# Performance work log

Hardware: AMD Instinct MI355X
Metric: run time of the kernel (lower is better)

Reference implementation:

```python
import jax, jax.numpy as jnp
import numpy as np

DILATION = 3
HC_MULT = 4
HIDDEN_DIM = 32
ENGRAM_DIM = 32
KERNEL_SIZE = 4
EPS = 1.1920929e-07  # torch RMSNorm default eps=None -> finfo(fp32).eps


def rmsnorm(x, w):
    # x: [..., C], w broadcastable to x
    ms = jnp.mean(x * x, axis=-1, keepdims=True)
    return x * jax.lax.rsqrt(ms + EPS) * w


def setup_inputs() -> dict:
    key = jax.random.key(0)
    ks = jax.random.split(key, 12)
    B, T = 16, 8192
    s = 0.05
    return {
        "embeddings": jax.random.normal(ks[0], (B, T, ENGRAM_DIM), jnp.float32),
        "hidden_states": jax.random.normal(ks[1], (B, T, HC_MULT, HIDDEN_DIM), jnp.float32),
        "Wv": jax.random.normal(ks[2], (HIDDEN_DIM, ENGRAM_DIM), jnp.float32) * s,
        "bv": jax.random.normal(ks[3], (HIDDEN_DIM,), jnp.float32) * s,
        "Wk": jax.random.normal(ks[4], (HC_MULT, HIDDEN_DIM, ENGRAM_DIM), jnp.float32) * s,
        "bk": jax.random.normal(ks[5], (HC_MULT, HIDDEN_DIM), jnp.float32) * s,
        "n1_w": jnp.ones((HC_MULT, HIDDEN_DIM), jnp.float32),
        "n2_w": jnp.ones((HC_MULT, HIDDEN_DIM), jnp.float32),
        "cn_w": jnp.ones((HC_MULT, HIDDEN_DIM), jnp.float32),
        "conv_w": jax.random.normal(ks[6], (HC_MULT * HIDDEN_DIM, 1, KERNEL_SIZE), jnp.float32) * s,
    }


def reference(embeddings, hidden_states, Wv, bv, Wk, bk, n1_w, n2_w, cn_w, conv_w):
    B, T, G, C = hidden_states.shape
    # per-branch key projection: [B,T,G,C]
    key = jnp.einsum("btd,gcd->btgc", embeddings, Wk) + bk
    normed_key = rmsnorm(key, n1_w)                    # [B,T,G,C]
    normed_query = rmsnorm(hidden_states, n2_w)        # [B,T,G,C]
    gate = jnp.sum(normed_key * normed_query, axis=-1) / np.sqrt(C)  # [B,T,G]
    gate = jnp.sqrt(jnp.maximum(jnp.abs(gate), 1e-6)) * jnp.sign(gate)
    gate = jax.nn.sigmoid(gate)[..., None]             # [B,T,G,1]
    value = (embeddings @ Wv.T + bv)[:, :, None, :]    # [B,T,1,C]
    gated = gate * value                               # [B,T,G,C]
    # per-branch RMSNorm then concat channels
    x_norm = rmsnorm(gated, cn_w).reshape(B, T, G * C)
    x_bct = jnp.transpose(x_norm, (0, 2, 1))           # [B, G*C, T]
    pad = (KERNEL_SIZE - 1) * DILATION                 # causal left pad = 9
    y_bct = jax.lax.conv_general_dilated(
        x_bct, conv_w,
        window_strides=(1,), padding=[(pad, 0)],
        rhs_dilation=(DILATION,),
        dimension_numbers=("NCH", "OIH", "NCH"),
        feature_group_count=G * C,
    )
    y_bct = jax.nn.silu(y_bct)
    conv_out = jnp.transpose(y_bct, (0, 2, 1)).reshape(B, T, G, C)
    return gated + conv_out
```

## Files before the change

kernel.cpp:

```cpp
#include <hip/hip_runtime.h>
#include <hip/hip_fp16.h>

#define TT    64
#define HALO  9
#define NTOK  73
#define XSTR  132
#define VSTR  36
#define EPS   1.1920929e-07f

#define GRID1  2048
#define NM     683
#define GRID2  4098

typedef __attribute__((ext_vector_type(8))) _Float16 f16x8;
typedef __attribute__((ext_vector_type(4))) float f32x4;

template<int CTRL>
__device__ __forceinline__ float dpp_add(float x) {
    int y = __builtin_amdgcn_update_dpp(0, __float_as_int(x), CTRL, 0xF, 0xF, true);
    return x + __int_as_float(y);
}
__device__ __forceinline__ float redsum16(float x) {
    x = dpp_add<0x128>(x);
    x = dpp_add<0x124>(x);
    x = dpp_add<0x122>(x);
    x = dpp_add<0x121>(x);
    return x;
}

__device__ __forceinline__ float fast_rcp(float x) {
    return __builtin_amdgcn_rcpf(x);
}

extern "C" __global__ __launch_bounds__(640)
void engram_prep(const float* __restrict__ Wv,
                 const float* __restrict__ Wk,
                 const float* __restrict__ n1w,
                 const float* __restrict__ n2w,
                 __half* __restrict__ wfrag,
                 float* __restrict__ w12)
{
    const int idx = threadIdx.x;
    if (idx < 128) w12[idx] = n1w[idx] * n2w[idx];
    const int nt  = idx >> 6;
    const int l15 = (idx >> 2) & 15;
    const int q   = idx & 3;
    const int e = nt & 1, p = nt >> 1;
    const int ch = 2 * l15 + e;
    const float* wrow = (p == 0) ? &Wv[ch * 32] : &Wk[((p - 1) * 32 + ch) * 32];
    float4 w0 = ((const float4*)wrow)[q * 2];
    float4 w1 = ((const float4*)wrow)[q * 2 + 1];
    __half2* dst = (__half2*)(wfrag + (size_t)idx * 8);
    dst[0] = __floats2half2_rn(w0.x, w0.y);
    dst[1] = __floats2half2_rn(w0.z, w0.w);
    dst[2] = __floats2half2_rn(w1.x, w1.y);
    dst[3] = __floats2half2_rn(w1.z, w1.w);
}

extern "C" __global__ __launch_bounds__(256, 1)
void engram_norm(const float* __restrict__ emb,
                 const float* __restrict__ hid,
                 const float* __restrict__ bv,
                 const float* __restrict__ bk,
                 const float* __restrict__ w12,
                 const float* __restrict__ cnw,
                 const __half* __restrict__ wfrag,
                 __half* __restrict__ xn_out,
                 float* __restrict__ val_out,
                 float* __restrict__ gate_out)
{
    const int tid  = threadIdx.x;
    const int b    = blockIdx.x >> 7;
    const int tile = blockIdx.x & 127;
    const int t0   = tile * 64;

    const int wv  = tid >> 6;
    const int ln  = tid & 63;
    const int l15 = ln & 15;
    const int q   = ln >> 4;
    const int tw  = t0 + wv * 16;

    float2 q2[4][4];
    #pragma unroll
    for (int r = 0; r < 4; ++r) {
        const int t = tw + q * 4 + r;
        const float2* qp = (const float2*)&hid[(size_t)((b << 13) + t) * 128];
        #pragma unroll
        for (int g = 0; g < 4; ++g) q2[r][g] = qp[g * 16 + l15];
    }

    float4 f0, f1;
    {
        const float4* p = (const float4*)&emb[(size_t)((b << 13) + tw + l15) * 32 + q * 8];
        f0 = p[0];
        f1 = p[1];
    }

    const float2 bv2 = ((const float2*)bv)[l15];
    float2 bk2[4], wnn[4], wcn[4];
    #pragma unroll
    for (int g = 0; g < 4; ++g) {
        bk2[g] = ((const float2*)(bk  + g * 32))[l15];
        wnn[g] = ((const float2*)(w12 + g * 32))[l15];
        wcn[g] = ((const float2*)(cnw + g * 32))[l15];
    }

    f16x8 a;
    a[0] = (_Float16)f0.x; a[1] = (_Float16)f0.y;
    a[2] = (_Float16)f0.z; a[3] = (_Float16)f0.w;
    a[4] = (_Float16)f1.x; a[5] = (_Float16)f1.y;
    a[6] = (_Float16)f1.z; a[7] = (_Float16)f1.w;

    const f16x8* wf = (const f16x8*)wfrag;
    f32x4 D[10];
    #pragma unroll
    for (int nt = 0; nt < 10; ++nt) {
        const int e = nt & 1, p = nt >> 1;
        f16x8 bf = wf[nt * 64 + l15 * 4 + q];
        const float bias = (p == 0) ? (e ? bv2.y : bv2.x)
                                    : (e ? bk2[p - 1].y : bk2[p - 1].x);
        f32x4 c = {bias, bias, bias, bias};
        D[nt] = __builtin_amdgcn_mfma_f32_16x16x32_f16(a, bf, c, 0, 0, 0);
    }

    #pragma unroll
    for (int r = 0; r < 4; ++r) {
        const int ti = tw + q * 4 + r;
        const float V0 = D[0][r], V1 = D[1][r];
        float msv = redsum16(V0 * V0 + V1 * V1);
        float gs[4];
        float xnv[4][2];
        #pragma unroll
        for (int g = 0; g < 4; ++g) {
            const float K0 = D[2 + 2 * g][r], K1v = D[3 + 2 * g][r];
            const float q0 = q2[r][g].x, q1 = q2[r][g].y;
            float msk = redsum16(K0 * K0 + K1v * K1v);
            float msq = redsum16(q0 * q0 + q1 * q1);
            float dr  = redsum16(K0 * wnn[g].x * q0 + K1v * wnn[g].y * q1);
            float rkq = rsqrtf((msk * (1.f / 32.f) + EPS) * (msq * (1.f / 32.f) + EPS));
            float dot = dr * rkq * 0.17677669529663689f;
            float sa = sqrtf(fmaxf(fabsf(dot), 1e-6f));
            float gate = fast_rcp(1.f + __expf(-copysignf(sa, dot)));
            gs[g] = gate;
            float sc = gate * rsqrtf(gate * gate * msv * (1.f / 32.f) + EPS);
            xnv[g][0] = sc * V0 * wcn[g].x;
            xnv[g][1] = sc * V1 * wcn[g].y;
        }
        __half* xrow = xn_out + (size_t)((b << 13) + ti) * 128;
        #pragma unroll
        for (int g = 0; g < 4; ++g) {
            *(__half2*)&xrow[g * 32 + 2 * l15] = __floats2half2_rn(xnv[g][0], xnv[g][1]);
        }
        *(float2*)&val_out[(size_t)((b << 13) + ti) * 32 + 2 * l15] = make_float2(V0, V1);
        if (l15 < 4) {
            float gsel = (l15 == 0) ? gs[0] : (l15 == 1) ? gs[1]
                       : (l15 == 2) ? gs[2] : gs[3];
            gate_out[(size_t)((b << 13) + ti) * 4 + l15] = gsel;
        }
    }
}

extern "C" __global__ __launch_bounds__(256, 1)
void engram_conv(const __half* __restrict__ xn,
                 const float* __restrict__ val,
                 const float* __restrict__ gate,
                 const float* __restrict__ cw,
                 float* __restrict__ out)
{
    const int gid = blockIdx.x * 256 + threadIdx.x;
    const int c4i = gid & 31;
    const int c4  = c4i << 2;
    const int g   = c4 >> 5;
    int rest = gid >> 5;
    const int m  = rest % NM;
    rest /= NM;
    const int r  = rest % 3;
    const int b  = rest / 3;
    const int t0 = 12 * m + r;

    const float4* cw4p = (const float4*)cw;
    const float4 w0 = cw4p[c4 + 0];
    const float4 w1 = cw4p[c4 + 1];
    const float4 w2 = cw4p[c4 + 2];
    const float4 w3 = cw4p[c4 + 3];

    float2 tap01[7], tap23[7];
    #pragma unroll
    for (int j = 0; j < 7; ++j) {
        const int tr = t0 - 9 + 3 * j;
        const float mj = (tr >= 0) ? 1.f : 0.f;
        const int trc = tr < 0 ? 0 : (tr > 8191 ? 8191 : tr);
        const __half2* xp = (const __half2*)&xn[(size_t)((b << 13) + trc) * 128 + c4];
        float2 a01 = __half22float2(xp[0]);
        float2 a23 = __half22float2(xp[1]);
        tap01[j] = make_float2(mj * a01.x, mj * a01.y);
        tap23[j] = make_float2(mj * a23.x, mj * a23.y);
    }

    #pragma unroll
    for (int i = 0; i < 4; ++i) {
        const int t = t0 + 3 * i;
        if (t < 8192) {
            float y0 = 0.f, y1 = 0.f, y2 = 0.f, y3 = 0.f;
            #pragma unroll
            for (int k = 0; k < 4; ++k) {
                const float wk0 = (k == 0) ? w0.x : (k == 1) ? w0.y : (k == 2) ? w0.z : w0.w;
                const float wk1 = (k == 0) ? w1.x : (k == 1) ? w1.y : (k == 2) ? w1.z : w1.w;
                const float wk2 = (k == 0) ? w2.x : (k == 1) ? w2.y : (k == 2) ? w2.z : w2.w;
                const float wk3 = (k == 0) ? w3.x : (k == 1) ? w3.y : (k == 2) ? w3.z : w3.w;
                y0 = fmaf(tap01[i + k].x, wk0, y0);
                y1 = fmaf(tap01[i + k].y, wk1, y1);
                y2 = fmaf(tap23[i + k].x, wk2, y2);
                y3 = fmaf(tap23[i + k].y, wk3, y3);
            }
            const size_t row = (size_t)((b << 13) + t);
            const float gg = gate[row * 4 + g];
            const f32x4 v  = *(const f32x4*)&val[row * 32 + (c4 & 31)];
            float4 o;
            o.x = gg * v[0] + y0 * fast_rcp(1.f + __expf(-y0));
            o.y = gg * v[1] + y1 * fast_rcp(1.f + __expf(-y1));
            o.z = gg * v[2] + y2 * fast_rcp(1.f + __expf(-y2));
            o.w = gg * v[3] + y3 * fast_rcp(1.f + __expf(-y3));
            *(float4*)&out[row * 128 + c4] = o;
        }
    }
}

extern "C" __global__ __launch_bounds__(320, 3)
void engram_fused(const float* __restrict__ emb,
                  const float* __restrict__ hid,
                  const float* __restrict__ Wv,
                  const float* __restrict__ bv,
                  const float* __restrict__ Wk,
                  const float* __restrict__ bk,
                  const float* __restrict__ n1w,
                  const float* __restrict__ n2w,
                  const float* __restrict__ cnw,
                  const float* __restrict__ cw,
                  float* __restrict__ out)
{
    __shared__ __align__(16) __half s_xn[NTOK * XSTR];
    __shared__ __align__(16) float  s_val[TT * VSTR];
    __shared__ float  s_gate[TT * 4];

    const int tid  = threadIdx.x;
    const int b    = blockIdx.x >> 7;
    const int tile = blockIdx.x & 127;
    const int t0   = tile * TT;

    const int wv  = tid >> 6;
    const int ln  = tid & 63;
    const int l15 = ln & 15;
    const int q   = ln >> 4;
    const int ibase = wv * 16 + q * 4;

    float2 q2[4][4];
    float  okm[4];
    #pragma unroll
    for (int r = 0; r < 4; ++r) {
        int t = t0 - HALO + ibase + r;
        okm[r] = (t >= 0 && t < 8192) ? 1.f : 0.f;
        int tc = t < 0 ? 0 : (t > 8191 ? 8191 : t);
        const float2* qp = (const float2*)&hid[(size_t)((b << 13) + tc) * 128];
        #pragma unroll
        for (int g = 0; g < 4; ++g) q2[r][g] = qp[g * 16 + l15];
    }

    float4 f0, f1;
    float amask;
    {
        const int tA = t0 - HALO + wv * 16 + l15;
        amask = (tA >= 0 && tA < 8192) ? 1.f : 0.f;
        const int tAc = tA < 0 ? 0 : (tA > 8191 ? 8191 : tA);
        const float4* p = (const float4*)&emb[(size_t)((b << 13) + tAc) * 32 + q * 8];
        f0 = p[0];
        f1 = p[1];
    }

    const float2 bv2 = ((const float2*)bv)[l15];
    float2 bk2[4], wn1[4], wn2[4], wcn[4];
    #pragma unroll
    for (int g = 0; g < 4; ++g) {
        bk2[g] = ((const float2*)(bk  + g * 32))[l15];
        wn1[g] = ((const float2*)(n1w + g * 32))[l15];
        wn2[g] = ((const float2*)(n2w + g * 32))[l15];
        wcn[g] = ((const float2*)(cnw + g * 32))[l15];
    }

    f16x8 a;
    a[0] = (_Float16)(amask * f0.x); a[1] = (_Float16)(amask * f0.y);
    a[2] = (_Float16)(amask * f0.z); a[3] = (_Float16)(amask * f0.w);
    a[4] = (_Float16)(amask * f1.x); a[5] = (_Float16)(amask * f1.y);
    a[6] = (_Float16)(amask * f1.z); a[7] = (_Float16)(amask * f1.w);

    f32x4 D[10];
    #pragma unroll
    for (int nt = 0; nt < 10; ++nt) {
        const int e = nt & 1, p = nt >> 1;
        const int ch = 2 * l15 + e;
        const float* wrow = (p == 0) ? &Wv[ch * 32] : &Wk[((p - 1) * 32 + ch) * 32];
        float4 w0 = ((const float4*)wrow)[q * 2];
        float4 w1 = ((const float4*)wrow)[q * 2 + 1];
        f16x8 bf;
        bf[0] = (_Float16)w0.x; bf[1] = (_Float16)w0.y;
        bf[2] = (_Float16)w0.z; bf[3] = (_Float16)w0.w;
        bf[4] = (_Float16)w1.x; bf[5] = (_Float16)w1.y;
        bf[6] = (_Float16)w1.z; bf[7] = (_Float16)w1.w;
        const float bias = (p == 0) ? (e ? bv2.y : bv2.x)
                                    : (e ? bk2[p - 1].y : bk2[p - 1].x);
        f32x4 c = {bias, bias, bias, bias};
        D[nt] = __builtin_amdgcn_mfma_f32_16x16x32_f16(a, bf, c, 0, 0, 0);
    }

    #pragma unroll
    for (int r = 0; r < 4; ++r) {
        const int i = ibase + r;
        const float V0 = D[0][r], V1 = D[1][r];
        float msv = redsum16(V0 * V0 + V1 * V1);
        float gs[4];
        float xnv[4][2];
        #pragma unroll
        for (int g = 0; g < 4; ++g) {
            const float K0 = D[2 + 2 * g][r], K1v = D[3 + 2 * g][r];
            const float q0 = q2[r][g].x * okm[r], q1 = q2[r][g].y * okm[r];
            float msk = redsum16(K0 * K0 + K1v * K1v);
            float msq = redsum16(q0 * q0 + q1 * q1);
            float dr  = redsum16(K0 * wn1[g].x * q0 * wn2[g].x
                               + K1v * wn1[g].y * q1 * wn2[g].y);
            float rk = rsqrtf(msk * (1.f / 32.f) + EPS);
            float rq = rsqrtf(msq * (1.f / 32.f) + EPS);
            float dot = dr * rk * rq * 0.17677669529663689f;
            float sa = sqrtf(fmaxf(fabsf(dot), 1e-6f));
            float gate = fast_rcp(1.f + __expf(-copysignf(sa, dot)));
            gs[g] = gate;
            float sc = gate * rsqrtf(gate * gate * msv * (1.f / 32.f) + EPS);
            xnv[g][0] = sc * V0 * wcn[g].x;
            xnv[g][1] = sc * V1 * wcn[g].y;
        }
        if (i < NTOK) {
            #pragma unroll
            for (int g = 0; g < 4; ++g) {
                __half2 h2 = __floats2half2_rn(okm[r] * xnv[g][0], okm[r] * xnv[g][1]);
                *(__half2*)&s_xn[i * XSTR + g * 32 + 2 * l15] = h2;
            }
            if (i >= HALO) {
                const int j = i - HALO;
                *(float2*)&s_val[j * VSTR + 2 * l15] = make_float2(V0, V1);
                if (l15 < 4) {
                    float gsel = (l15 == 0) ? gs[0] : (l15 == 1) ? gs[1]
                               : (l15 == 2) ? gs[2] : gs[3];
                    s_gate[j * 4 + l15] = gsel;
                }
            }
        }
    }
    __syncthreads();

    const float4* cw4p = (const float4*)cw;
    for (int idx = tid; idx < TT * 32; idx += 320) {
        const int j  = idx >> 5;
        const int c4 = (idx & 31) << 2;
        float4 w0 = cw4p[c4 + 0];
        float4 w1 = cw4p[c4 + 1];
        float4 w2 = cw4p[c4 + 2];
        float4 w3 = cw4p[c4 + 3];
        float y0 = 0.f, y1 = 0.f, y2 = 0.f, y3 = 0.f;
        #pragma unroll
        for (int k = 0; k < 4; ++k) {
            const __half2* xp = (const __half2*)&s_xn[(j + 3 * k) * XSTR + c4];
            float2 a01 = __half22float2(xp[0]);
            float2 a23 = __half22float2(xp[1]);
            const float wk0 = (k == 0) ? w0.x : (k == 1) ? w0.y : (k == 2) ? w0.z : w0.w;
            const float wk1 = (k == 0) ? w1.x : (k == 1) ? w1.y : (k == 2) ? w1.z : w1.w;
            const float wk2 = (k == 0) ? w2.x : (k == 1) ? w2.y : (k == 2) ? w2.z : w2.w;
            const float wk3 = (k == 0) ? w3.x : (k == 1) ? w3.y : (k == 2) ? w3.z : w3.w;
            y0 = fmaf(a01.x, wk0, y0);
            y1 = fmaf(a01.y, wk1, y1);
            y2 = fmaf(a23.x, wk2, y2);
            y3 = fmaf(a23.y, wk3, y3);
        }
        const float g  = s_gate[j * 4 + (c4 >> 5)];
        const f32x4 v  = *(const f32x4*)&s_val[j * VSTR + (c4 & 31)];
        float4 o;
        o.x = g * v[0] + y0 * fast_rcp(1.f + __expf(-y0));
        o.y = g * v[1] + y1 * fast_rcp(1.f + __expf(-y1));
        o.z = g * v[2] + y2 * fast_rcp(1.f + __expf(-y2));
        o.w = g * v[3] + y3 * fast_rcp(1.f + __expf(-y3));
        *(float4*)&out[(size_t)((b << 13) + t0 + j) * 128 + c4] = o;
    }
}

extern "C" void kernel_launch(void* const* d_in, const int* in_sizes, int n_in,
                              void* d_out, int out_size, void* d_ws, size_t ws_size,
                              hipStream_t stream) {
    const float* emb = (const float*)d_in[0];
    const float* hid = (const float*)d_in[1];
    const float* Wv  = (const float*)d_in[2];
    const float* bvp = (const float*)d_in[3];
    const float* Wk  = (const float*)d_in[4];
    const float* bkp = (const float*)d_in[5];
    const float* n1  = (const float*)d_in[6];
    const float* n2  = (const float*)d_in[7];
    const float* cn  = (const float*)d_in[8];
    const float* cwp = (const float*)d_in[9];
    float* out = (float*)d_out;

    const size_t xn_bytes   = (size_t)16 * 8192 * 128 * sizeof(__half);
    const size_t val_bytes  = (size_t)16 * 8192 * 32 * sizeof(float);
    const size_t gate_bytes = (size_t)16 * 8192 * 4 * sizeof(float);
    const size_t wf_bytes   = (size_t)640 * 8 * sizeof(__half);
    const size_t w12_bytes  = (size_t)128 * sizeof(float);
    const size_t need = xn_bytes + val_bytes + gate_bytes + wf_bytes + w12_bytes;

    if (d_ws != nullptr && ws_size >= need) {
        __half* xn  = (__half*)d_ws;
        float* val  = (float*)((char*)d_ws + xn_bytes);
        float* gate = (float*)((char*)d_ws + xn_bytes + val_bytes);
        __half* wf  = (__half*)((char*)d_ws + xn_bytes + val_bytes + gate_bytes);
        float* w12  = (float*)((char*)d_ws + xn_bytes + val_bytes + gate_bytes + wf_bytes);
        engram_prep<<<dim3(1), dim3(640), 0, stream>>>(Wv, Wk, n1, n2, wf, w12);
        engram_norm<<<dim3(GRID1), dim3(256), 0, stream>>>(
            emb, hid, bvp, bkp, w12, cn, wf, xn, val, gate);
        engram_conv<<<dim3(GRID2), dim3(256), 0, stream>>>(
            xn, val, gate, cwp, out);
    } else {
        engram_fused<<<dim3(16 * 128), dim3(320), 0, stream>>>(
            emb, hid, Wv, bvp, Wk, bkp, n1, n2, cn, cwp, out);
    }
}
```

Baseline: 165.7 us.

## Transpose MFMA operands so each lane owns one token's channels

The weight fragments are relaid so the weights become the A operand and the embeddings the B operand. Each lane then holds four consecutive channels of a single token. Per-token reductions become mostly in-register FMAs followed by two cross-lane steps (swizzle plus bpermute), replacing 16-lane DPP reductions, and stores become wider vectors. This cuts the number of shuffle instructions and store transactions in the norm kernel, at the cost of loading float4 bias and norm weights per lane.

```diff
diff --git a/kernel.cpp b/kernel.cpp
--- a/kernel.cpp
+++ b/kernel.cpp
@@ -25,6 +25,14 @@
     x = dpp_add<0x124>(x);
     x = dpp_add<0x122>(x);
     x = dpp_add<0x121>(x);
+    return x;
+}
+
+__device__ __forceinline__ float redq(float x, int a32) {
+    int y = __builtin_amdgcn_ds_swizzle(__float_as_int(x), 0x401F);
+    x += __int_as_float(y);
+    y = __builtin_amdgcn_ds_bpermute(a32, __float_as_int(x));
+    x += __int_as_float(y);
     return x;
 }
 
@@ -43,13 +51,14 @@
     const int idx = threadIdx.x;
     if (idx < 128) w12[idx] = n1w[idx] * n2w[idx];
     const int nt  = idx >> 6;
-    const int l15 = (idx >> 2) & 15;
-    const int q   = idx & 3;
-    const int e = nt & 1, p = nt >> 1;
-    const int ch = 2 * l15 + e;
+    const int lnp = idx & 63;
+    const int l15 = lnp & 15;
+    const int q   = lnp >> 4;
+    const int h = nt & 1, p = nt >> 1;
+    const int ch = h * 16 + l15;
     const float* wrow = (p == 0) ? &Wv[ch * 32] : &Wk[((p - 1) * 32 + ch) * 32];
-    float4 w0 = ((const float4*)wrow)[q * 2];
-    float4 w1 = ((const float4*)wrow)[q * 2 + 1];
+    float4 w0 = ((const float4*)wrow)[2 * q];
+    float4 w1 = ((const float4*)wrow)[2 * q + 1];
     __half2* dst = (__half2*)(wfrag + (size_t)idx * 8);
     dst[0] = __floats2half2_rn(w0.x, w0.y);
     dst[1] = __floats2half2_rn(w0.z, w0.w);
@@ -79,84 +88,102 @@
     const int l15 = ln & 15;
     const int q   = ln >> 4;
     const int tw  = t0 + wv * 16;
-
-    float2 q2[4][4];
-    #pragma unroll
-    for (int r = 0; r < 4; ++r) {
-        const int t = tw + q * 4 + r;
-        const float2* qp = (const float2*)&hid[(size_t)((b << 13) + t) * 128];
-        #pragma unroll
-        for (int g = 0; g < 4; ++g) q2[r][g] = qp[g * 16 + l15];
-    }
-
-    float4 f0, f1;
-    {
-        const float4* p = (const float4*)&emb[(size_t)((b << 13) + tw + l15) * 32 + q * 8];
-        f0 = p[0];
-        f1 = p[1];
-    }
-
-    const float2 bv2 = ((const float2*)bv)[l15];
-    float2 bk2[4], wnn[4], wcn[4];
+    const int tok = tw + l15;
+    const size_t row = (size_t)((b << 13) + tok);
+    const int a32 = ((ln ^ 32) << 2);
+
+    float4 hq[4][2];
+    const float4* hp = (const float4*)&hid[row * 128];
     #pragma unroll
     for (int g = 0; g < 4; ++g) {
-        bk2[g] = ((const float2*)(bk  + g * 32))[l15];
-        wnn[g] = ((const float2*)(w12 + g * 32))[l15];
-        wcn[g] = ((const float2*)(cnw + g * 32))[l15];
-    }
-
-    f16x8 a;
-    a[0] = (_Float16)f0.x; a[1] = (_Float16)f0.y;
-    a[2] = (_Float16)f0.z; a[3] = (_Float16)f0.w;
-    a[4] = (_Float16)f1.x; a[5] = (_Float16)f1.y;
-    a[6] = (_Float16)f1.z; a[7] = (_Float16)f1.w;
+        hq[g][0] = hp[g * 8 + q];
+        hq[g][1] = hp[g * 8 + q + 4];
+    }
+
+    const float4* ep = (const float4*)&emb[row * 32];
+    const float4 e0 = ep[2 * q];
+    const float4 e1 = ep[2 * q + 1];
+    f16x8 bfe;
+    bfe[0] = (_Float16)e0.x; bfe[1] = (_Float16)e0.y;
+    bfe[2] = (_Float16)e0.z; bfe[3] = (_Float16)e0.w;
+    bfe[4] = (_Float16)e1.x; bfe[5] = (_Float16)e1.y;
+    bfe[6] = (_Float16)e1.z; bfe[7] = (_Float16)e1.w;
 
     const f16x8* wf = (const f16x8*)wfrag;
     f32x4 D[10];
     #pragma unroll
     for (int nt = 0; nt < 10; ++nt) {
-        const int e = nt & 1, p = nt >> 1;
-        f16x8 bf = wf[nt * 64 + l15 * 4 + q];
-        const float bias = (p == 0) ? (e ? bv2.y : bv2.x)
-                                    : (e ? bk2[p - 1].y : bk2[p - 1].x);
-        f32x4 c = {bias, bias, bias, bias};
-        D[nt] = __builtin_amdgcn_mfma_f32_16x16x32_f16(a, bf, c, 0, 0, 0);
-    }
-
-    #pragma unroll
-    for (int r = 0; r < 4; ++r) {
-        const int ti = tw + q * 4 + r;
-        const float V0 = D[0][r], V1 = D[1][r];
-        float msv = redsum16(V0 * V0 + V1 * V1);
-        float gs[4];
-        float xnv[4][2];
-        #pragma unroll
-        for (int g = 0; g < 4; ++g) {
-            const float K0 = D[2 + 2 * g][r], K1v = D[3 + 2 * g][r];
-            const float q0 = q2[r][g].x, q1 = q2[r][g].y;
-            float msk = redsum16(K0 * K0 + K1v * K1v);
-            float msq = redsum16(q0 * q0 + q1 * q1);
-            float dr  = redsum16(K0 * wnn[g].x * q0 + K1v * wnn[g].y * q1);
-            float rkq = rsqrtf((msk * (1.f / 32.f) + EPS) * (msq * (1.f / 32.f) + EPS));
-            float dot = dr * rkq * 0.17677669529663689f;
-            float sa = sqrtf(fmaxf(fabsf(dot), 1e-6f));
-            float gate = fast_rcp(1.f + __expf(-copysignf(sa, dot)));
-            gs[g] = gate;
-            float sc = gate * rsqrtf(gate * gate * msv * (1.f / 32.f) + EPS);
-            xnv[g][0] = sc * V0 * wcn[g].x;
-            xnv[g][1] = sc * V1 * wcn[g].y;
-        }
-        __half* xrow = xn_out + (size_t)((b << 13) + ti) * 128;
-        #pragma unroll
-        for (int g = 0; g < 4; ++g) {
-            *(__half2*)&xrow[g * 32 + 2 * l15] = __floats2half2_rn(xnv[g][0], xnv[g][1]);
-        }
-        *(float2*)&val_out[(size_t)((b << 13) + ti) * 32 + 2 * l15] = make_float2(V0, V1);
-        if (l15 < 4) {
-            float gsel = (l15 == 0) ? gs[0] : (l15 == 1) ? gs[1]
-                       : (l15 == 2) ? gs[2] : gs[3];
-            gate_out[(size_t)((b << 13) + ti) * 4 + l15] = gsel;
-        }
+        const int h = nt & 1, p = nt >> 1;
+        f16x8 af = wf[nt * 64 + ln];
+        float4 bias = (p == 0) ? ((const float4*)bv)[h * 4 + q]
+                               : ((const float4*)bk)[(p - 1) * 8 + h * 4 + q];
+        f32x4 c = {bias.x, bias.y, bias.z, bias.w};
+        D[nt] = __builtin_amdgcn_mfma_f32_16x16x32_f16(af, bfe, c, 0, 0, 0);
+    }
+
+    const f32x4 Va = D[0], Vb = D[1];
+    float msv;
+    {
+        float s = Va[0] * Va[0];
+        s = fmaf(Va[1], Va[1], s); s = fmaf(Va[2], Va[2], s); s = fmaf(Va[3], Va[3], s);
+        s = fmaf(Vb[0], Vb[0], s); s = fmaf(Vb[1], Vb[1], s);
+        s = fmaf(Vb[2], Vb[2], s); s = fmaf(Vb[3], Vb[3], s);
+        msv = redq(s, a32);
+    }
+
+    __half* xrow = xn_out + row * 128;
+    float* vrow  = val_out + row * 32;
+    float gs[4];
+    #pragma unroll
+    for (int g = 0; g < 4; ++g) {
+        const f32x4 Ka = D[2 + 2 * g], Kb = D[3 + 2 * g];
+        const float4 qa = hq[g][0], qb = hq[g][1];
+        const float4 wa = ((const float4*)(w12 + g * 32))[q];
+        const float4 wb = ((const float4*)(w12 + g * 32))[q + 4];
+
+        float msk = Ka[0] * Ka[0];
+        msk = fmaf(Ka[1], Ka[1], msk); msk = fmaf(Ka[2], Ka[2], msk); msk = fmaf(Ka[3], Ka[3], msk);
+        msk = fmaf(Kb[0], Kb[0], msk); msk = fmaf(Kb[1], Kb[1], msk);
+        msk = fmaf(Kb[2], Kb[2], msk); msk = fmaf(Kb[3], Kb[3], msk);
+
+        float msq = qa.x * qa.x;
+        msq = fmaf(qa.y, qa.y, msq); msq = fmaf(qa.z, qa.z, msq); msq = fmaf(qa.w, qa.w, msq);
+        msq = fmaf(qb.x, qb.x, msq); msq = fmaf(qb.y, qb.y, msq);
+        msq = fmaf(qb.z, qb.z, msq); msq = fmaf(qb.w, qb.w, msq);
+
+        float dr = (Ka[0] * wa.x) * qa.x;
+        dr = fmaf(Ka[1] * wa.y, qa.y, dr); dr = fmaf(Ka[2] * wa.z, qa.z, dr);
+        dr = fmaf(Ka[3] * wa.w, qa.w, dr);
+        dr = fmaf(Kb[0] * wb.x, qb.x, dr); dr = fmaf(Kb[1] * wb.y, qb.y, dr);
+        dr = fmaf(Kb[2] * wb.z, qb.z, dr); dr = fmaf(Kb[3] * wb.w, qb.w, dr);
+
+        msk = redq(msk, a32);
+        msq = redq(msq, a32);
+        dr  = redq(dr,  a32);
+
+        float rkq = rsqrtf((msk * (1.f / 32.f) + EPS) * (msq * (1.f / 32.f) + EPS));
+        float dot = rkq * dr * 0.17677669529663689f;
+        float sa = sqrtf(fmaxf(fabsf(dot), 1e-6f));
+        float gate = fast_rcp(1.f + __expf(-copysignf(sa, dot)));
+        gs[g] = gate;
+        float sc = gate * rsqrtf(gate * gate * msv * (1.f / 32.f) + EPS);
+
+        const float4 ca = ((const float4*)(cnw + g * 32))[q];
+        const float4 cb = ((const float4*)(cnw + g * 32))[q + 4];
+        __half2 ha[2], hb[2];
+        ha[0] = __floats2half2_rn(sc * Va[0] * ca.x, sc * Va[1] * ca.y);
+        ha[1] = __floats2half2_rn(sc * Va[2] * ca.z, sc * Va[3] * ca.w);
+        hb[0] = __floats2half2_rn(sc * Vb[0] * cb.x, sc * Vb[1] * cb.y);
+        hb[1] = __floats2half2_rn(sc * Vb[2] * cb.z, sc * Vb[3] * cb.w);
+        *(float2*)&xrow[g * 32 + q * 4]      = *(float2*)ha;
+        *(float2*)&xrow[g * 32 + 16 + q * 4] = *(float2*)hb;
+    }
+
+    *(f32x4*)&vrow[q * 4]      = Va;
+    *(f32x4*)&vrow[16 + q * 4] = Vb;
+    {
+        float gsel = (q == 0) ? gs[0] : (q == 1) ? gs[1] : (q == 2) ? gs[2] : gs[3];
+        gate_out[row * 4 + q] = gsel;
     }
 }
 
```

Result: slower. 175.7 us (+6.0%).
